# Performance work log

Measured on AMD Instinct MI355X. Metric: run time of the kernel, lower is better.

## Reference

```python
import jax, jax.numpy as jnp
import numpy as np

D = 1024      # model_dim
H = 16        # num_heads
HD = D // H   # head_size
B = 4
S = 2048


def setup_inputs() -> dict:
    key = jax.random.key(0)
    ks = jax.random.split(key, 6)
    sc = 1.0 / np.sqrt(D)
    embedded = jax.random.normal(ks[0], (B, S, D), dtype=jnp.float32)
    # Per-head projection weights stacked: [H, D, HD] (nn.Linear, bias=False)
    Wq = jax.random.normal(ks[1], (H, D, HD), dtype=jnp.float32) * sc
    Wk = jax.random.normal(ks[2], (H, D, HD), dtype=jnp.float32) * sc
    Wv = jax.random.normal(ks[3], (H, D, HD), dtype=jnp.float32) * sc
    # Output projection nn.Linear(D, D) with bias
    Wo = jax.random.normal(ks[4], (D, D), dtype=jnp.float32) * sc
    bo = jax.random.normal(ks[5], (D,), dtype=jnp.float32) * sc
    return {"embedded": embedded, "Wq": Wq, "Wk": Wk, "Wv": Wv, "Wo": Wo, "bo": bo}


def reference(embedded, Wq, Wk, Wv, Wo, bo):
    # q,k,v: [B, H, S, HD]
    q = jnp.einsum('bsd,hde->bhse', embedded, Wq)
    k = jnp.einsum('bsd,hde->bhse', embedded, Wk)
    v = jnp.einsum('bsd,hde->bhse', embedded, Wv)
    scores = jnp.einsum('bhse,bhte->bhst', q, k) / jnp.sqrt(jnp.float32(HD))
    causal = jnp.tril(jnp.ones((S, S), dtype=bool))  # [S, S]
    scores = jnp.where(causal, scores, -jnp.inf)
    attn = jax.nn.softmax(scores, axis=-1)
    ctx = jnp.einsum('bhst,bhte->bhse', attn, v)  # [B, H, S, HD]
    # concat heads -> [B, S, D]
    concat = jnp.transpose(ctx, (0, 2, 1, 3)).reshape(B, S, D)
    # dropout=0.0 -> identity
    return concat @ Wo.T + bo
```

## Files before the change

### kernel.cpp

```cpp
#include <hip/hip_runtime.h>
#include <hip/hip_bf16.h>
#include <stdint.h>
#include <stddef.h>

typedef __bf16 bf16;
typedef __bf16 bf16x4 __attribute__((ext_vector_type(4)));
typedef __bf16 bf16x8 __attribute__((ext_vector_type(8)));
typedef float f32x4 __attribute__((ext_vector_type(4)));
typedef float f32x16 __attribute__((ext_vector_type(16)));


__device__ __forceinline__ void gload16(const void* g, void* lds) {
  __builtin_amdgcn_global_load_lds(
      (const __attribute__((address_space(1))) unsigned int*)(uintptr_t)g,
      (__attribute__((address_space(3))) unsigned int*)(unsigned int)(uintptr_t)lds,
      16, 0, 0);
}

__device__ __forceinline__ bf16x8 lds_read8(const bf16* base, int row, int slot) {
  const char* p = (const char*)base + row * 128 + ((slot ^ (row & 7)) << 4);
  return *(const bf16x8*)p;
}


__global__ void k_cvt(const float* __restrict__ emb, const float* __restrict__ Wq,
                      const float* __restrict__ Wk, const float* __restrict__ Wv,
                      const float* __restrict__ Wo, bf16* __restrict__ E,
                      bf16* __restrict__ WT, bf16* __restrict__ WoB) {
  if (blockIdx.x < 4096) {
    int i = blockIdx.x * blockDim.x + threadIdx.x;
    const float4* s4 = (const float4*)emb;
    float4 a = s4[2 * i], b = s4[2 * i + 1];
    bf16x8 v;
    v[0] = (bf16)a.x; v[1] = (bf16)a.y; v[2] = (bf16)a.z; v[3] = (bf16)a.w;
    v[4] = (bf16)b.x; v[5] = (bf16)b.y; v[6] = (bf16)b.z; v[7] = (bf16)b.w;
    ((bf16x8*)E)[i] = v;
  } else {
    int i = (blockIdx.x - 4096) * blockDim.x + threadIdx.x;
    if (i < 16 * 192 * 1024) {
      int h = i / (192 * 1024);
      int rem = i - h * (192 * 1024);
      int r = rem >> 10;
      int d = rem & 1023;
      const float* W = (r < 64) ? Wq : (r < 128 ? Wk : Wv);
      int e = r & 63;
      WT[i] = (bf16)W[h * 65536 + d * 64 + e];
    } else {
      int j = i - 16 * 192 * 1024;
      WoB[j] = (bf16)Wo[j];
    }
  }
}


__launch_bounds__(256, 2)
__global__ void k_qkv(const bf16* __restrict__ E, const bf16* __restrict__ WT,
                      bf16* __restrict__ Qo, bf16* __restrict__ Ko, bf16* __restrict__ Vt) {
  __shared__ __align__(16) bf16 As[2][128 * 64];
  __shared__ __align__(16) bf16 Bs[2][192 * 64];
  const int h = blockIdx.x;
  const int m0 = blockIdx.y * 128;
  const int tid = threadIdx.x;
  const int w = tid >> 6, lane = tid & 63;
  const int wm = w >> 1, wn = w & 1;
  const int cl = lane & 15, g4 = lane >> 4;
  const int srow = lane >> 3;
  const int scol = ((lane & 7) ^ (lane >> 3)) << 3;
  const bf16* Wh = WT + (size_t)h * 192 * 1024;
  f32x4 zero = {0.f, 0.f, 0.f, 0.f};
  f32x4 acc[4][6];
#pragma unroll
  for (int m = 0; m < 4; ++m)
#pragma unroll
    for (int n = 0; n < 6; ++n) acc[m][n] = zero;

  auto stage = [&](int kt, int buf) {
    const int k0 = kt * 64;
#pragma unroll
    for (int c = 0; c < 4; ++c) {
      int cc = w * 4 + c;
      gload16(E + (size_t)(m0 + cc * 8 + srow) * 1024 + k0 + scol, (char*)As[buf] + cc * 1024);
    }
#pragma unroll
    for (int c = 0; c < 6; ++c) {
      int cc = w * 6 + c;
      gload16(Wh + (size_t)(cc * 8 + srow) * 1024 + k0 + scol, (char*)Bs[buf] + cc * 1024);
    }
  };

  stage(0, 0);
  int cur = 0;
  for (int kt = 0; kt < 16; ++kt) {
    __syncthreads();
    if (kt + 1 < 16) stage(kt + 1, cur ^ 1);
#pragma unroll
    for (int kk = 0; kk < 2; ++kk) {
      bf16x8 a[4], b[6];
#pragma unroll
      for (int m = 0; m < 4; ++m) a[m] = lds_read8(As[cur], wm * 64 + m * 16 + cl, kk * 4 + g4);
#pragma unroll
      for (int n = 0; n < 6; ++n) b[n] = lds_read8(Bs[cur], wn * 96 + n * 16 + cl, kk * 4 + g4);
#pragma unroll
      for (int m = 0; m < 4; ++m)
#pragma unroll
        for (int n = 0; n < 6; ++n)
          acc[m][n] = __builtin_amdgcn_mfma_f32_16x16x32_bf16(a[m], b[n], acc[m][n], 0, 0, 0);
    }
    cur ^= 1;
  }
#pragma unroll
  for (int n = 0; n < 6; ++n) {
    int ncol = wn * 96 + n * 16 + cl;
    int which = ncol >> 6, e = ncol & 63;
    if (which == 2) {
#pragma unroll
      for (int m = 0; m < 4; ++m) {
        int row = m0 + wm * 64 + m * 16 + g4 * 4;
        int bb = row >> 11, ss = row & 2047;
        bf16x4 vv;
#pragma unroll
        for (int r = 0; r < 4; ++r) vv[r] = (bf16)acc[m][n][r];
        *(bf16x4*)(Vt + ((size_t)(bb * 16 + h) * 64 + e) * 2048 + ss) = vv;
      }
    } else {
      bf16* dst = (which == 0) ? Qo : Ko;
      const float sc = (which == 0) ? 0.18033688f : 1.0f;
#pragma unroll
      for (int m = 0; m < 4; ++m) {
#pragma unroll
        for (int r = 0; r < 4; ++r) {
          int row = m0 + wm * 64 + m * 16 + g4 * 4 + r;
          int bb = row >> 11, ss = row & 2047;
          dst[(((size_t)(bb * 16 + h) * 2048 + ss) << 6) + e] = (bf16)(acc[m][n][r] * sc);
        }
      }
    }
  }
}


__launch_bounds__(512)
__global__ void k_attn(const bf16* __restrict__ Qg, const bf16* __restrict__ Kg,
                       const bf16* __restrict__ Vtg, bf16* __restrict__ CTX) {
  __shared__ __align__(16) bf16 KS[2][8192];
  __shared__ __align__(16) bf16 VT[2][8192];
  const int b = blockIdx.x;
  const int bh = b & 63;
  const int g = b >> 6;
  const int qt = (g < 4) ? g : 11 - g;
  const int q0 = qt * 256;
  const int tid = threadIdx.x, w = tid >> 6, lane = tid & 63;
  const int ql = lane & 31, hi = lane >> 5;
  const int q = q0 + 32 * w + ql;
  const int qmin = q0 + 32 * w;
  const int qmax = qmin + 31;
  const bf16* Qb = Qg + (size_t)bh * (2048 * 64);
  const bf16* Kb = Kg + (size_t)bh * (2048 * 64);
  const bf16* Vb = Vtg + (size_t)bh * (64 * 2048);
  const int ntk = 2 * qt + 2;

  bf16x8 qf[4];
#pragma unroll
  for (int ks = 0; ks < 4; ++ks)
    qf[ks] = *(const bf16x8*)(Qb + (size_t)q * 64 + ks * 16 + hi * 8);

  f32x16 o0, o1;
#pragma unroll
  for (int i = 0; i < 16; ++i) { o0[i] = 0.f; o1[i] = 0.f; }
  float ls = 0.f;

  const int srowK = w * 8 + (lane >> 3);
  const int phiRow = (srowK & ~12) | ((srowK & 4) << 1) | ((srowK & 8) >> 1);
  const int scolK = ((lane & 7) ^ ((lane >> 3) & 7)) << 3;
  const int vrow0 = w * 4 + (lane >> 4);
  const int vkey0 = ((lane & 15) ^ (vrow0 & 7)) * 8;
  const int vrow1 = 32 + vrow0;
  const int vkey1 = ((lane & 15) ^ (vrow1 & 7)) * 8;
  int offs[4];
#pragma unroll
  for (int ks = 0; ks < 4; ++ks) offs[ks] = (ks * 32 + hi * 16) ^ ((ql & 7) << 4);

  auto stage = [&](int kv, int buf) {
    gload16(Kb + (size_t)(kv + phiRow) * 64 + scolK, (char*)KS[buf] + w * 1024);
    gload16(Kb + (size_t)(kv + 64 + phiRow) * 64 + scolK, (char*)KS[buf] + 8192 + w * 1024);
    gload16(Vb + (size_t)vrow0 * 2048 + kv + vkey0, (char*)VT[buf] + w * 1024);
    gload16(Vb + (size_t)vrow1 * 2048 + kv + vkey1, (char*)VT[buf] + 8192 + w * 1024);
  };

  auto do_half = [&](int kv0h, const char* kbase, const char* vtb, int halfB) {
    f32x16 s0, s1;
#pragma unroll
    for (int i = 0; i < 16; ++i) { s0[i] = 0.f; s1[i] = 0.f; }
    __builtin_amdgcn_s_setprio(1);
#pragma unroll
    for (int ks = 0; ks < 4; ++ks) {
      bf16x8 k0 = *(const bf16x8*)(kbase + ql * 128 + offs[ks]);
      bf16x8 k1 = *(const bf16x8*)(kbase + (32 + ql) * 128 + offs[ks]);
      s0 = __builtin_amdgcn_mfma_f32_32x32x16_bf16(k0, qf[ks], s0, 0, 0, 0);
      s1 = __builtin_amdgcn_mfma_f32_32x32x16_bf16(k1, qf[ks], s1, 0, 0, 0);
    }
    __builtin_amdgcn_s_setprio(0);
    if (kv0h + 63 > qmin) {
      int dqh = q - kv0h - 8 * hi;
#pragma unroll
      for (int r = 0; r < 16; ++r) {
        const int c0 = (r & 7) + ((r & 8) << 1);
        if (c0 > dqh) s0[r] = -1e30f;
        if (c0 + 32 > dqh) s1[r] = -1e30f;
      }
    }
#pragma unroll
    for (int i = 0; i < 16; ++i) {
      s0[i] = exp2f(s0[i]);
      s1[i] = exp2f(s1[i]);
    }
    bf16x8 pf[4];
#pragma unroll
    for (int j = 0; j < 8; ++j) {
      pf[0][j] = (bf16)s0[j];
      pf[1][j] = (bf16)s0[8 + j];
      pf[2][j] = (bf16)s1[j];
      pf[3][j] = (bf16)s1[8 + j];
    }
    __builtin_amdgcn_s_setprio(1);
#pragma unroll
    for (int ks = 0; ks < 4; ++ks) {
      bf16x8 v0 = *(const bf16x8*)(vtb + ql * 256 + halfB + offs[ks]);
      bf16x8 v1 = *(const bf16x8*)(vtb + (32 + ql) * 256 + halfB + offs[ks]);
      o0 = __builtin_amdgcn_mfma_f32_32x32x16_bf16(v0, pf[ks], o0, 0, 0, 0);
      o1 = __builtin_amdgcn_mfma_f32_32x32x16_bf16(v1, pf[ks], o1, 0, 0, 0);
    }
    __builtin_amdgcn_s_setprio(0);
    float a8[8];
#pragma unroll
    for (int i = 0; i < 8; ++i) a8[i] = (s0[i] + s0[i + 8]) + (s1[i] + s1[i + 8]);
    ls += ((a8[0] + a8[1]) + (a8[2] + a8[3])) + ((a8[4] + a8[5]) + (a8[6] + a8[7]));
  };

  stage(0, 0);
  int cur = 0;
  for (int t = 0; t < ntk; ++t) {
    const int kv0 = t * 128;
    __syncthreads();
    if (t + 1 < ntk) stage(kv0 + 128, cur ^ 1);
    if (kv0 <= qmax)
      do_half(kv0, (const char*)KS[cur], (const char*)VT[cur], 0);
    if (kv0 + 64 <= qmax)
      do_half(kv0 + 64, (const char*)KS[cur] + 8192, (const char*)VT[cur], 128);
    cur ^= 1;
  }

  ls += __shfl_xor(ls, 32);
  const float inv = 1.0f / ls;
  const int bb = bh >> 4, hh = bh & 15;
  bf16* Cp = CTX + ((size_t)(bb * 2048 + q) * 1024) + hh * 64;
#pragma unroll
  for (int r = 0; r < 16; ++r) {
    int d0 = (r & 3) + 8 * (r >> 2) + 4 * hi;
    Cp[d0] = (bf16)(o0[r] * inv);
    Cp[32 + d0] = (bf16)(o1[r] * inv);
  }
}


__launch_bounds__(256, 2)
__global__ void k_oproj(const bf16* __restrict__ X, const bf16* __restrict__ Wb,
                        const float* __restrict__ bo, float* __restrict__ out) {
  __shared__ __align__(16) bf16 As[2][128 * 64];
  __shared__ __align__(16) bf16 Bs[2][128 * 64];
  const int m0 = blockIdx.x * 128, n0 = blockIdx.y * 128;
  const int tid = threadIdx.x, w = tid >> 6, lane = tid & 63;
  const int wm = w >> 1, wn = w & 1;
  const int cl = lane & 15, g4 = lane >> 4;
  const int srow = lane >> 3;
  const int scol = ((lane & 7) ^ (lane >> 3)) << 3;
  f32x4 zero = {0.f, 0.f, 0.f, 0.f};
  f32x4 acc[4][4];
#pragma unroll
  for (int m = 0; m < 4; ++m)
#pragma unroll
    for (int n = 0; n < 4; ++n) acc[m][n] = zero;

  auto stage = [&](int kt, int buf) {
    const int k0 = kt * 64;
#pragma unroll
    for (int c = 0; c < 4; ++c) {
      int cc = w * 4 + c;
      gload16(X + (size_t)(m0 + cc * 8 + srow) * 1024 + k0 + scol, (char*)As[buf] + cc * 1024);
      gload16(Wb + (size_t)(n0 + cc * 8 + srow) * 1024 + k0 + scol, (char*)Bs[buf] + cc * 1024);
    }
  };

  stage(0, 0);
  int cur = 0;
  for (int kt = 0; kt < 16; ++kt) {
    __syncthreads();
    if (kt + 1 < 16) stage(kt + 1, cur ^ 1);
#pragma unroll
    for (int kk = 0; kk < 2; ++kk) {
      bf16x8 a[4], b[4];
#pragma unroll
      for (int m = 0; m < 4; ++m) a[m] = lds_read8(As[cur], wm * 64 + m * 16 + cl, kk * 4 + g4);
#pragma unroll
      for (int n = 0; n < 4; ++n) b[n] = lds_read8(Bs[cur], wn * 64 + n * 16 + cl, kk * 4 + g4);
#pragma unroll
      for (int m = 0; m < 4; ++m)
#pragma unroll
        for (int n = 0; n < 4; ++n)
          acc[m][n] = __builtin_amdgcn_mfma_f32_16x16x32_bf16(a[m], b[n], acc[m][n], 0, 0, 0);
    }
    cur ^= 1;
  }
#pragma unroll
  for (int n = 0; n < 4; ++n) {
    int col = n0 + wn * 64 + n * 16 + cl;
    float bias = bo[col];
#pragma unroll
    for (int m = 0; m < 4; ++m)
#pragma unroll
      for (int r = 0; r < 4; ++r) {
        int row = m0 + wm * 64 + m * 16 + g4 * 4 + r;
        out[(size_t)row * 1024 + col] = acc[m][n][r] + bias;
      }
  }
}


extern "C" void kernel_launch(void* const* d_in, const int* in_sizes, int n_in,
                              void* d_out, int out_size, void* d_ws, size_t ws_size,
                              hipStream_t stream) {
  const float* emb = (const float*)d_in[0];
  const float* Wq  = (const float*)d_in[1];
  const float* Wk  = (const float*)d_in[2];
  const float* Wv  = (const float*)d_in[3];
  const float* Wo  = (const float*)d_in[4];
  const float* bo  = (const float*)d_in[5];
  float* out = (float*)d_out;

  const size_t NEED = (size_t)72 << 20;
  if (ws_size < NEED) return;

  char* ws = (char*)d_ws;
  bf16* E   = (bf16*)(ws);
  bf16* WT  = (bf16*)(ws + ((size_t)16 << 20));
  bf16* WoB = (bf16*)(ws + ((size_t)22 << 20));
  bf16* Qw  = (bf16*)(ws + ((size_t)24 << 20));
  bf16* Kw  = (bf16*)(ws + ((size_t)40 << 20));
  bf16* Vtw = (bf16*)(ws + ((size_t)56 << 20));
  bf16* CTX = E;

  k_cvt<<<20480, 256, 0, stream>>>(emb, Wq, Wk, Wv, Wo, E, WT, WoB);
  k_qkv<<<dim3(16, 64), 256, 0, stream>>>(E, WT, Qw, Kw, Vtw);
  k_attn<<<512, 512, 0, stream>>>(Qw, Kw, Vtw, CTX);
  k_oproj<<<dim3(64, 8), 256, 0, stream>>>(CTX, WoB, bo, out);
}
```

Measured before the change: 156.0 us.

## Split long causal attention tiles across blocks and merge partials in a combine kernel

Causal attention work is rebalanced so each of the 512 blocks does about nine KV steps. The long query tiles (4–7) are split into two KV ranges, and the second half is paired with a short query tile in the same block. Partial unnormalised outputs and row sums go to workspace and are merged by a new combine kernel. This removes the load imbalance of the causal triangle, at the cost of an extra launch, extra global traffic for the partials, and a bf16 rounding of the partial sums. Merging the partials works without max rescaling because the kernel never tracks a running max.

```diff
diff --git a/kernel.cpp b/kernel.cpp
--- a/kernel.cpp
+++ b/kernel.cpp
@@ -139,25 +139,40 @@
 }
 
 
+template <int MODE>
 __launch_bounds__(512)
 __global__ void k_attn(const bf16* __restrict__ Qg, const bf16* __restrict__ Kg,
-                       const bf16* __restrict__ Vtg, bf16* __restrict__ CTX) {
+                       const bf16* __restrict__ Vtg, bf16* __restrict__ CTX,
+                       bf16* __restrict__ PO, float* __restrict__ LS) {
   __shared__ __align__(16) bf16 KS[2][8192];
   __shared__ __align__(16) bf16 VT[2][8192];
   const int b = blockIdx.x;
   const int bh = b & 63;
   const int g = b >> 6;
-  const int qt = (g < 4) ? g : 11 - g;
-  const int q0 = qt * 256;
   const int tid = threadIdx.x, w = tid >> 6, lane = tid & 63;
   const int ql = lane & 31, hi = lane >> 5;
-  const int q = q0 + 32 * w + ql;
-  const int qmin = q0 + 32 * w;
-  const int qmax = qmin + 31;
   const bf16* Qb = Qg + (size_t)bh * (2048 * 64);
   const bf16* Kb = Kg + (size_t)bh * (2048 * 64);
   const bf16* Vb = Vtg + (size_t)bh * (64 * 2048);
-  const int ntk = 2 * qt + 2;
+
+  int qtA, tA0, lenA, slotA, qtB, lenB, hasB;
+  if (MODE == 0) {
+    qtA = (g < 4) ? g : 11 - g; tA0 = 0; lenA = 2 * qtA + 2;
+    hasB = 0; slotA = -1; qtB = 0; lenB = 0;
+  } else {
+    const int e = g >> 1, odd = g & 1;
+    qtA = 7 - e;
+    tA0 = odd ? 9 : 0;
+    lenA = odd ? (2 * qtA + 2 - 9) : 9;
+    slotA = (qtA - 4) * 2 + odd;
+    hasB = odd; qtB = e; lenB = 2 * e + 2;
+  }
+  const int nstep = lenA + (hasB ? lenB : 0);
+
+  int qt = qtA;
+  int q = qt * 256 + 32 * w + ql;
+  int qmin = qt * 256 + 32 * w;
+  int qmax = qmin + 31;
 
   bf16x8 qf[4];
 #pragma unroll
@@ -180,6 +195,10 @@
 #pragma unroll
   for (int ks = 0; ks < 4; ++ks) offs[ks] = (ks * 32 + hi * 16) ^ ((ql & 7) << 4);
 
+  auto stepkv = [&](int i) -> int {
+    return (i < lenA) ? (tA0 + i) * 128 : (i - lenA) * 128;
+  };
+
   auto stage = [&](int kv, int buf) {
     gload16(Kb + (size_t)(kv + phiRow) * 64 + scolK, (char*)KS[buf] + w * 1024);
     gload16(Kb + (size_t)(kv + 64 + phiRow) * 64 + scolK, (char*)KS[buf] + 8192 + w * 1024);
@@ -237,12 +256,38 @@
     ls += ((a8[0] + a8[1]) + (a8[2] + a8[3])) + ((a8[4] + a8[5]) + (a8[6] + a8[7]));
   };
 
-  stage(0, 0);
+  auto flushPartial = [&]() {
+    float l2 = ls + __shfl_xor(ls, 32);
+    const int row = 32 * w + ql;
+    if (hi == 0) LS[(slotA * 64 + bh) * 256 + row] = l2;
+    bf16* Pp = PO + (((size_t)slotA * 64 + bh) * 256 + row) * 64;
+#pragma unroll
+    for (int r = 0; r < 16; ++r) {
+      int d0 = (r & 3) + 8 * (r >> 2) + 4 * hi;
+      Pp[d0] = (bf16)o0[r];
+      Pp[32 + d0] = (bf16)o1[r];
+    }
+  };
+
+  stage(stepkv(0), 0);
   int cur = 0;
-  for (int t = 0; t < ntk; ++t) {
-    const int kv0 = t * 128;
+  for (int i = 0; i < nstep; ++i) {
     __syncthreads();
-    if (t + 1 < ntk) stage(kv0 + 128, cur ^ 1);
+    if (i + 1 < nstep) stage(stepkv(i + 1), cur ^ 1);
+    if (MODE == 1 && hasB && i == lenA) {
+      flushPartial();
+      qt = qtB;
+      q = qt * 256 + 32 * w + ql;
+      qmin = qt * 256 + 32 * w;
+      qmax = qmin + 31;
+#pragma unroll
+      for (int ks = 0; ks < 4; ++ks)
+        qf[ks] = *(const bf16x8*)(Qb + (size_t)q * 64 + ks * 16 + hi * 8);
+#pragma unroll
+      for (int j = 0; j < 16; ++j) { o0[j] = 0.f; o1[j] = 0.f; }
+      ls = 0.f;
+    }
+    const int kv0 = stepkv(i);
     if (kv0 <= qmax)
       do_half(kv0, (const char*)KS[cur], (const char*)VT[cur], 0);
     if (kv0 + 64 <= qmax)
@@ -250,15 +295,47 @@
     cur ^= 1;
   }
 
-  ls += __shfl_xor(ls, 32);
-  const float inv = 1.0f / ls;
+  if (MODE == 1 && !hasB) {
+    flushPartial();
+  } else {
+    float l2 = ls + __shfl_xor(ls, 32);
+    const float inv = 1.0f / l2;
+    const int bb = bh >> 4, hh = bh & 15;
+    bf16* Cp = CTX + ((size_t)(bb * 2048 + q) * 1024) + hh * 64;
+#pragma unroll
+    for (int r = 0; r < 16; ++r) {
+      int d0 = (r & 3) + 8 * (r >> 2) + 4 * hi;
+      Cp[d0] = (bf16)(o0[r] * inv);
+      Cp[32 + d0] = (bf16)(o1[r] * inv);
+    }
+  }
+}
+
+
+__launch_bounds__(512)
+__global__ void k_comb(const bf16* __restrict__ PO, const float* __restrict__ LS,
+                       bf16* __restrict__ CTX) {
+  const int t = blockIdx.x;
+  const int qtp = t >> 6, bh = t & 63;
+  const int qt = qtp + 4;
   const int bb = bh >> 4, hh = bh & 15;
-  bf16* Cp = CTX + ((size_t)(bb * 2048 + q) * 1024) + hh * 64;
-#pragma unroll
-  for (int r = 0; r < 16; ++r) {
-    int d0 = (r & 3) + 8 * (r >> 2) + 4 * hi;
-    Cp[d0] = (bf16)(o0[r] * inv);
-    Cp[32 + d0] = (bf16)(o1[r] * inv);
+  const int tid = threadIdx.x;
+  const int r = tid >> 1, dh = (tid & 1) * 32;
+  const int s0 = qtp * 2, s1 = qtp * 2 + 1;
+  float la = LS[(s0 * 64 + bh) * 256 + r];
+  float lb = LS[(s1 * 64 + bh) * 256 + r];
+  float inv = 1.0f / (la + lb);
+  const bf16* A = PO + (((size_t)s0 * 64 + bh) * 256 + r) * 64 + dh;
+  const bf16* B = PO + (((size_t)s1 * 64 + bh) * 256 + r) * 64 + dh;
+  bf16* C = CTX + ((size_t)(bb * 2048 + qt * 256 + r) * 1024) + hh * 64 + dh;
+#pragma unroll
+  for (int j = 0; j < 32; j += 8) {
+    bf16x8 a = *(const bf16x8*)(A + j);
+    bf16x8 b = *(const bf16x8*)(B + j);
+    bf16x8 o;
+#pragma unroll
+    for (int k = 0; k < 8; ++k) o[k] = (bf16)(((float)a[k] + (float)b[k]) * inv);
+    *(bf16x8*)(C + j) = o;
   }
 }
 
@@ -337,8 +414,9 @@
   const float* bo  = (const float*)d_in[5];
   float* out = (float*)d_out;
 
-  const size_t NEED = (size_t)72 << 20;
-  if (ws_size < NEED) return;
+  const size_t NEED_BASE  = (size_t)72 << 20;
+  const size_t NEED_SPLIT = (size_t)90 << 20;
+  if (ws_size < NEED_BASE) return;
 
   char* ws = (char*)d_ws;
   bf16* E   = (bf16*)(ws);
@@ -347,10 +425,17 @@
   bf16* Qw  = (bf16*)(ws + ((size_t)24 << 20));
   bf16* Kw  = (bf16*)(ws + ((size_t)40 << 20));
   bf16* Vtw = (bf16*)(ws + ((size_t)56 << 20));
+  bf16* PO  = (bf16*)(ws + ((size_t)72 << 20));
+  float* LS = (float*)(ws + ((size_t)88 << 20));
   bf16* CTX = E;
 
   k_cvt<<<20480, 256, 0, stream>>>(emb, Wq, Wk, Wv, Wo, E, WT, WoB);
   k_qkv<<<dim3(16, 64), 256, 0, stream>>>(E, WT, Qw, Kw, Vtw);
-  k_attn<<<512, 512, 0, stream>>>(Qw, Kw, Vtw, CTX);
+  if (ws_size >= NEED_SPLIT) {
+    k_attn<1><<<512, 512, 0, stream>>>(Qw, Kw, Vtw, CTX, PO, LS);
+    k_comb<<<256, 512, 0, stream>>>(PO, LS, CTX);
+  } else {
+    k_attn<0><<<512, 512, 0, stream>>>(Qw, Kw, Vtw, CTX, PO, LS);
+  }
   k_oproj<<<dim3(64, 8), 256, 0, stream>>>(CTX, WoB, bo, out);
 }
```

Measured after the change: 170.0 us. 9.0% more time.
